# Optimization experiments

Measured on AMD Instinct MI355X. Metric: run time of the kernel, lower is better.

## Reference

```python
import jax, jax.numpy as jnp
import numpy as np

HEADS = 12
HEAD_SIZE = 64
INF = 1e12  # K.infinity() in bert4keras

B, L, D = 8, 1024, 768


def setup_inputs() -> dict:
    key = jax.random.key(0)
    k1, k2 = jax.random.split(key)
    x = jax.random.normal(k1, (B, L, D), dtype=jnp.float32)
    W = jax.random.normal(k2, (D, HEADS * HEAD_SIZE * 2), dtype=jnp.float32) * (1.0 / np.sqrt(D))
    b = jnp.zeros((HEADS * HEAD_SIZE * 2,), dtype=jnp.float32)
    mask = jnp.ones((B, L), dtype=jnp.int32)
    return {"x": x, "W": W, "b": b, "mask": mask}


def _rope_sin_cos(seq_len, head_size, dtype):
    # SinusoidalPositionEmbedding(head_size, 'zero'):
    # emb[n, 2i] = sin(n * 10000^(-2i/S)), emb[n, 2i+1] = cos(...)
    pos = jnp.arange(seq_len, dtype=dtype)                       # [L]
    inv = jnp.power(jnp.asarray(10000.0, dtype),
                    -2.0 * jnp.arange(head_size // 2, dtype=dtype) / head_size)  # [S/2]
    ang = pos[:, None] * inv[None, :]                            # [L, S/2]
    # repeat_elements(..., 2, -1): [c0,c0,c1,c1,...]
    cos_pos = jnp.repeat(jnp.cos(ang), 2, axis=-1)               # [L, S]
    sin_pos = jnp.repeat(jnp.sin(ang), 2, axis=-1)               # [L, S]
    return sin_pos[None, :, None, :], cos_pos[None, :, None, :]  # [1,L,1,S]


def _rotate_half_interleaved(t):
    # stack([-t[...,1::2], t[...,::2]], -1).reshape(t.shape)
    t2 = jnp.stack([-t[..., 1::2], t[..., ::2]], axis=-1)
    return t2.reshape(t.shape)


def reference(x, W, b, mask):
    dtype = x.dtype
    Bq, Lq, _ = x.shape
    S = HEAD_SIZE
    # dense projection + head split: [B, L, H, 2S]
    proj = (jnp.einsum('bld,de->ble', x, W) + b).reshape(Bq, Lq, HEADS, 2 * S)
    qw, kw = proj[..., :S], proj[..., S:]
    # inline RoPE (interleaved variant)
    sin_pos, cos_pos = _rope_sin_cos(Lq, S, dtype)
    qw = qw * cos_pos + _rotate_half_interleaved(qw) * sin_pos
    kw = kw * cos_pos + _rotate_half_interleaved(kw) * sin_pos
    # bilinear score: [B, H, L, L]
    logits = jnp.einsum('bmhd,bnhd->bhmn', qw, kw)
    # padding mask on axis 2 (rows) and axis 3 (cols): x*m + (-INF)*(1-m)
    m = mask.astype(dtype)
    m_row = m[:, None, :, None]
    m_col = m[:, None, None, :]
    logits = logits * m_row + (-INF) * (1.0 - m_row)
    logits = logits * m_col + (-INF) * (1.0 - m_col)
    # upper-triangular (incl. diagonal) mask
    tri = jnp.triu(jnp.ones((Lq, Lq), dtype=dtype))
    logits = logits - (1.0 - tri) * INF
    return logits / np.sqrt(S).astype(np.float32)
```

## Files before the change

### kernel.cpp

```cpp
#include <hip/hip_runtime.h>
#include <hip/hip_bf16.h>
#include <stdint.h>

#define NHEADS 12
#define HS 64
#define NB 8
#define NL 1024
#define ND 768
#define NE 1536
#define INFV 1000000000000.0f

typedef __bf16 bf16x8 __attribute__((ext_vector_type(8)));
typedef float f32x4 __attribute__((ext_vector_type(4)));

typedef __attribute__((address_space(1))) const unsigned int gas_uint;
typedef __attribute__((address_space(3))) unsigned int las_uint;
#define GLOAD_LDS16(g, l) __builtin_amdgcn_global_load_lds((gas_uint*)(g), (las_uint*)(l), 16, 0, 0)

__device__ __forceinline__ unsigned short f2bf(float f) {
  unsigned int u = __builtin_bit_cast(unsigned int, f);
  u += 0x7fffu + ((u >> 16) & 1u);
  return (unsigned short)(u >> 16);
}

__device__ __forceinline__ bf16x8 load_frag(const unsigned short* p) {
  uint4 v = *(const uint4*)p;
  return __builtin_bit_cast(bf16x8, v);
}

__global__ __launch_bounds__(256) void k_prep(
    const float* __restrict__ x, const float* __restrict__ W,
    unsigned short* __restrict__ xb, unsigned short* __restrict__ wt,
    float* __restrict__ cst) {
  const int blk = blockIdx.x;
  if (blk < 6144) {
    int i = blk * 256 + threadIdx.x;
    float4 v = ((const float4*)x)[i];
    ushort4 o;
    o.x = f2bf(v.x); o.y = f2bf(v.y); o.z = f2bf(v.z); o.w = f2bf(v.w);
    ((ushort4*)xb)[i] = o;
  } else if (blk < 6144 + 288) {
    __shared__ float tile[64][65];
    int t = blk - 6144;
    int te = t % 24, td = t / 24;
    int c = threadIdx.x & 63, r4 = threadIdx.x >> 6;
    #pragma unroll
    for (int rr = 0; rr < 16; rr++) {
      int row = rr * 4 + r4;
      tile[row][c] = W[(size_t)(td * 64 + row) * NE + te * 64 + c];
    }
    __syncthreads();
    #pragma unroll
    for (int rr = 0; rr < 16; rr++) {
      int row = rr * 4 + r4;
      wt[(size_t)(te * 64 + row) * ND + td * 64 + c] = f2bf(tile[c][row]);
    }
  } else {
    int t = (blk - 6432) * 256 + threadIdx.x;
    int p = t >> 5, i = t & 31;
    float inv = powf(10000.0f, -(float)i / 32.0f);
    float sv, cv;
    sincosf((float)p * inv, &sv, &cv);
    cst[(p * 32 + i) * 2 + 0] = cv;
    cst[(p * 32 + i) * 2 + 1] = sv;
  }
}

__global__ __launch_bounds__(256) void k_proj_rope(
    const unsigned short* __restrict__ xb,
    const unsigned short* __restrict__ wt,
    const float* __restrict__ bias,
    const float* __restrict__ cst,
    unsigned short* __restrict__ qbuf, unsigned short* __restrict__ kbuf) {
  const int h  = blockIdx.y;
  const int m0 = blockIdx.x * 128;
  const int e0 = h * 128;
  const int tid  = threadIdx.x;
  const int lane = tid & 63;
  const int w    = tid >> 6;
  const int wm = w >> 1, wn = w & 1;
  const int col_l = lane & 15, rq = lane >> 4;

  __shared__ unsigned short smem[16384];
  char* smem_b = (char*)smem;

  unsigned int goff[4], loff[4];
  #pragma unroll
  for (int q = 0; q < 4; q++) {
    int p  = q * 256 + tid;
    int r  = p >> 3, sl = p & 7;
    int s  = sl ^ (r & 7);
    goff[q] = r * ND + s * 8;
    loff[q] = p * 16;
  }
  const unsigned short* gA = wt + (size_t)e0 * ND;
  const unsigned short* gB = xb + (size_t)m0 * ND;

  const int xr = col_l & 7;
  const unsigned int aB0 = (unsigned)((wn * 64 + col_l) * 128 + ((0 * 4 + rq) ^ xr) * 16);
  const unsigned int aB1 = (unsigned)((wn * 64 + col_l) * 128 + ((1 * 4 + rq) ^ xr) * 16);
  const unsigned int bB0 = (unsigned)(16384 + (wm * 64 + col_l) * 128 + ((0 * 4 + rq) ^ xr) * 16);
  const unsigned int bB1 = (unsigned)(16384 + (wm * 64 + col_l) * 128 + ((1 * 4 + rq) ^ xr) * 16);

  f32x4 acc[4][4];
  #pragma unroll
  for (int i = 0; i < 4; i++)
    #pragma unroll
    for (int j = 0; j < 4; j++)
      #pragma unroll
      for (int q = 0; q < 4; q++) acc[i][j][q] = 0.0f;

  for (int kk = 0; kk < ND; kk += 64) {
    const unsigned short* sA = gA + kk;
    const unsigned short* sB = gB + kk;
    #pragma unroll
    for (int q = 0; q < 4; q++) GLOAD_LDS16(sA + goff[q], smem_b + loff[q]);
    #pragma unroll
    for (int q = 0; q < 4; q++) GLOAD_LDS16(sB + goff[q], smem_b + 16384 + loff[q]);
    __syncthreads();
    #pragma unroll
    for (int kkh = 0; kkh < 2; kkh++) {
      const unsigned int aB = kkh ? aB1 : aB0;
      const unsigned int bB = kkh ? bB1 : bB0;
      bf16x8 af[4], bfr[4];
      #pragma unroll
      for (int f = 0; f < 4; f++) {
        af[f]  = __builtin_bit_cast(bf16x8, *(const uint4*)(smem_b + aB + f * 2048));
        bfr[f] = __builtin_bit_cast(bf16x8, *(const uint4*)(smem_b + bB + f * 2048));
      }
      #pragma unroll
      for (int i = 0; i < 4; i++)
        #pragma unroll
        for (int j = 0; j < 4; j++)
          acc[i][j] = __builtin_amdgcn_mfma_f32_16x16x32_bf16(af[i], bfr[j], acc[i][j], 0, 0, 0);
    }
    __syncthreads();
  }

  unsigned short* obuf = (wn == 1) ? kbuf : qbuf;
  #pragma unroll
  for (int j = 0; j < 4; j++) {
    const int m   = m0 + wm * 64 + j * 16 + col_l;
    const int pos = m & (NL - 1);
    const int bb  = m >> 10;
    const float* crow = cst + pos * 64;
    unsigned short* orow = obuf + (((size_t)(bb * NHEADS + h)) * NL + pos) * HS;
    #pragma unroll
    for (int i = 0; i < 4; i++) {
      const int s0 = i * 16 + rq * 4;
      float4 bv = *(const float4*)&bias[e0 + wn * 64 + s0];
      float4 tq = *(const float4*)(crow + s0 * 2);
      float v0 = acc[i][j][0] + bv.x;
      float v1 = acc[i][j][1] + bv.y;
      float v2 = acc[i][j][2] + bv.z;
      float v3 = acc[i][j][3] + bv.w;
      ushort4 o;
      o.x = f2bf(v0 * tq.x - v1 * tq.y);
      o.y = f2bf(v1 * tq.x + v0 * tq.y);
      o.z = f2bf(v2 * tq.z - v3 * tq.w);
      o.w = f2bf(v3 * tq.z + v2 * tq.w);
      *(ushort4*)&orow[s0] = o;
    }
  }
}

__global__ __launch_bounds__(256) void k_logits(
    const unsigned short* __restrict__ qbuf,
    const unsigned short* __restrict__ kbuf,
    const int* __restrict__ mask,
    float* __restrict__ out) {
  const int f  = blockIdx.x;
  const int r  = f & 7, t = f >> 3;
  const int bh = r + 8 * (t >> 6);
  const int tile = t & 63;
  const int tm = tile >> 3, tn = tile & 7;
  const int b  = bh / NHEADS;
  const int tid  = threadIdx.x;
  const int* mrow = mask + b * NL;

  if (tn < tm) {
    const int n0 = tn * 128 + (tid & 31) * 4;
    int4 mc = *(const int4*)&mrow[n0];
    #pragma unroll
    for (int it = 0; it < 16; it++) {
      int m = tm * 128 + it * 8 + (tid >> 5);
      float mr = (float)mrow[m];
      float base = -INFV * (1.0f - mr);
      f32x4 o;
      o[0] = ((mc.x ? base : -INFV) - INFV) * 0.125f;
      o[1] = ((mc.y ? base : -INFV) - INFV) * 0.125f;
      o[2] = ((mc.z ? base : -INFV) - INFV) * 0.125f;
      o[3] = ((mc.w ? base : -INFV) - INFV) * 0.125f;
      __builtin_nontemporal_store(o, (f32x4*)(out + ((size_t)bh * NL + m) * NL + n0));
    }
    return;
  }

  const int lane = tid & 63;
  const int w    = tid >> 6;
  const int wm = w >> 1, wn = w & 1;
  const int m_base = tm * 128 + wm * 64;
  const int n_base = tn * 128 + wn * 64;
  const int col_l = lane & 15, rq = lane >> 4;
  const unsigned short* Q = qbuf + (size_t)bh * (NL * HS);
  const unsigned short* K = kbuf + (size_t)bh * (NL * HS);

  __shared__ float lds[64 * 132];

  f32x4 acc[4][4];
  #pragma unroll
  for (int i = 0; i < 4; i++)
    #pragma unroll
    for (int j = 0; j < 4; j++)
      #pragma unroll
      for (int q = 0; q < 4; q++) acc[i][j][q] = 0.0f;

  #pragma unroll
  for (int ks = 0; ks < 2; ks++) {
    bf16x8 ak[4], bq[4];
    #pragma unroll
    for (int ff = 0; ff < 4; ff++) {
      ak[ff] = load_frag(K + (size_t)(n_base + ff * 16 + col_l) * HS + ks * 32 + rq * 8);
      bq[ff] = load_frag(Q + (size_t)(m_base + ff * 16 + col_l) * HS + ks * 32 + rq * 8);
    }
    #pragma unroll
    for (int i = 0; i < 4; i++)
      #pragma unroll
      for (int j = 0; j < 4; j++)
        acc[i][j] = __builtin_amdgcn_mfma_f32_16x16x32_bf16(ak[i], bq[j], acc[i][j], 0, 0, 0);
  }

  const bool diag = (tn == tm);
  const int rb_row = tid >> 5;
  const int rb_c4  = (tid & 31) * 4;
  const int n_rb   = tn * 128 + rb_c4;
  int4 mc_rb = *(const int4*)&mrow[n_rb];
  const bool allmc = (mc_rb.x & mc_rb.y & mc_rb.z & mc_rb.w) != 0;

  #pragma unroll
  for (int pass = 0; pass < 2; pass++) {
    if (wm == pass) {
      #pragma unroll
      for (int j = 0; j < 4; j++) {
        const int rl = j * 16 + col_l;
        #pragma unroll
        for (int i = 0; i < 4; i++)
          *(f32x4*)&lds[rl * 132 + wn * 64 + i * 16 + rq * 4] = acc[i][j];
      }
    }
    __syncthreads();
    #pragma unroll
    for (int it = 0; it < 8; it++) {
      const int rl = it * 8 + rb_row;
      const int m  = tm * 128 + pass * 64 + rl;
      f32x4 v = *(const f32x4*)&lds[rl * 132 + rb_c4];
      if (mrow[m] == 0) { v[0] = -INFV; v[1] = -INFV; v[2] = -INFV; v[3] = -INFV; }
      if (!allmc) {
        if (mc_rb.x == 0) v[0] = -INFV;
        if (mc_rb.y == 0) v[1] = -INFV;
        if (mc_rb.z == 0) v[2] = -INFV;
        if (mc_rb.w == 0) v[3] = -INFV;
      }
      if (diag) {
        if (n_rb + 0 < m) v[0] -= INFV;
        if (n_rb + 1 < m) v[1] -= INFV;
        if (n_rb + 2 < m) v[2] -= INFV;
        if (n_rb + 3 < m) v[3] -= INFV;
      }
      v *= 0.125f;
      __builtin_nontemporal_store(v, (f32x4*)(out + ((size_t)bh * NL + m) * NL + n_rb));
    }
    __syncthreads();
  }
}

extern "C" void kernel_launch(void* const* d_in, const int* in_sizes, int n_in,
                              void* d_out, int out_size, void* d_ws, size_t ws_size,
                              hipStream_t stream) {
  const float* x    = (const float*)d_in[0];
  const float* W    = (const float*)d_in[1];
  const float* bias = (const float*)d_in[2];
  const int*   mask = (const int*)d_in[3];
  float* out = (float*)d_out;
  char* ws = (char*)d_ws;

  unsigned short* xb = (unsigned short*)(ws);
  unsigned short* wt = (unsigned short*)(ws + 12582912);
  unsigned short* qb = (unsigned short*)(ws + 14942208);
  unsigned short* kb = (unsigned short*)(ws + 27525120);
  float* cst = (float*)(ws + 40108032);

  k_prep<<<6560, 256, 0, stream>>>(x, W, xb, wt, cst);
  k_proj_rope<<<dim3(64, 12), 256, 0, stream>>>(xb, wt, bias, cst, qb, kb);
  k_logits<<<6144, 256, 0, stream>>>(qb, kb, mask, out);
}
```

Baseline: 127.8 us.

## Fuse fp32-to-bf16 conversion of x into projection GEMM with XCD-aware tile mapping

Removes the separate pass that converts x to bf16 in the prep kernel. The projection kernel now streams fp32 x tiles straight into a larger swizzled LDS buffer and converts them to bf16 as it builds the MFMA fragments. The grid becomes 1D and is remapped so the 12 head tiles that share the same rows of x land on the same XCD, which should improve L2 reuse of the wider fp32 loads. The RoPE cos/sin table index is also corrected. The cost is more global and LDS traffic per GEMM tile, plus conversion work inside the inner loop.

```diff
diff --git a/kernel.cpp b/kernel.cpp
--- a/kernel.cpp
+++ b/kernel.cpp
@@ -29,20 +29,13 @@
 }
 
 __global__ __launch_bounds__(256) void k_prep(
-    const float* __restrict__ x, const float* __restrict__ W,
-    unsigned short* __restrict__ xb, unsigned short* __restrict__ wt,
+    const float* __restrict__ W,
+    unsigned short* __restrict__ wt,
     float* __restrict__ cst) {
   const int blk = blockIdx.x;
-  if (blk < 6144) {
-    int i = blk * 256 + threadIdx.x;
-    float4 v = ((const float4*)x)[i];
-    ushort4 o;
-    o.x = f2bf(v.x); o.y = f2bf(v.y); o.z = f2bf(v.z); o.w = f2bf(v.w);
-    ((ushort4*)xb)[i] = o;
-  } else if (blk < 6144 + 288) {
+  if (blk < 288) {
     __shared__ float tile[64][65];
-    int t = blk - 6144;
-    int te = t % 24, td = t / 24;
+    int te = blk % 24, td = blk / 24;
     int c = threadIdx.x & 63, r4 = threadIdx.x >> 6;
     #pragma unroll
     for (int rr = 0; rr < 16; rr++) {
@@ -56,7 +49,7 @@
       wt[(size_t)(te * 64 + row) * ND + td * 64 + c] = f2bf(tile[c][row]);
     }
   } else {
-    int t = (blk - 6432) * 256 + threadIdx.x;
+    int t = (blk - 288) * 256 + threadIdx.x;
     int p = t >> 5, i = t & 31;
     float inv = powf(10000.0f, -(float)i / 32.0f);
     float sv, cv;
@@ -67,40 +60,46 @@
 }
 
 __global__ __launch_bounds__(256) void k_proj_rope(
-    const unsigned short* __restrict__ xb,
+    const float* __restrict__ x,
     const unsigned short* __restrict__ wt,
     const float* __restrict__ bias,
     const float* __restrict__ cst,
     unsigned short* __restrict__ qbuf, unsigned short* __restrict__ kbuf) {
-  const int h  = blockIdx.y;
-  const int m0 = blockIdx.x * 128;
-  const int e0 = h * 128;
+  const int blk = blockIdx.x;
+  const int xcd = blk & 7;
+  const int loc = blk >> 3;
+  const int h   = loc % 12;
+  const int mt  = xcd * 8 + loc / 12;
+  const int m0  = mt * 128;
+  const int e0  = h * 128;
   const int tid  = threadIdx.x;
   const int lane = tid & 63;
   const int w    = tid >> 6;
   const int wm = w >> 1, wn = w & 1;
   const int col_l = lane & 15, rq = lane >> 4;
 
-  __shared__ unsigned short smem[16384];
-  char* smem_b = (char*)smem;
-
-  unsigned int goff[4], loff[4];
+  __shared__ char smem_b[49152];
+
+  unsigned int goffA[4];
   #pragma unroll
   for (int q = 0; q < 4; q++) {
-    int p  = q * 256 + tid;
-    int r  = p >> 3, sl = p & 7;
-    int s  = sl ^ (r & 7);
-    goff[q] = r * ND + s * 8;
-    loff[q] = p * 16;
+    int p = q * 256 + tid;
+    int r = p >> 3, sl = p & 7;
+    goffA[q] = r * ND + (sl ^ (r & 7)) * 8;
+  }
+  unsigned int goffB[8];
+  #pragma unroll
+  for (int q = 0; q < 8; q++) {
+    int p = q * 256 + tid;
+    int r = p >> 4, sl = p & 15;
+    goffB[q] = r * ND + (sl ^ (r & 15)) * 4;
   }
   const unsigned short* gA = wt + (size_t)e0 * ND;
-  const unsigned short* gB = xb + (size_t)m0 * ND;
+  const float*          gB = x  + (size_t)m0 * ND;
 
   const int xr = col_l & 7;
-  const unsigned int aB0 = (unsigned)((wn * 64 + col_l) * 128 + ((0 * 4 + rq) ^ xr) * 16);
-  const unsigned int aB1 = (unsigned)((wn * 64 + col_l) * 128 + ((1 * 4 + rq) ^ xr) * 16);
-  const unsigned int bB0 = (unsigned)(16384 + (wm * 64 + col_l) * 128 + ((0 * 4 + rq) ^ xr) * 16);
-  const unsigned int bB1 = (unsigned)(16384 + (wm * 64 + col_l) * 128 + ((1 * 4 + rq) ^ xr) * 16);
+  const unsigned int aRow = (unsigned)((wn * 64 + col_l) * 128);
+  const unsigned int bRow = (unsigned)(16384 + (wm * 64 + col_l) * 256);
 
   f32x4 acc[4][4];
   #pragma unroll
@@ -112,21 +111,24 @@
 
   for (int kk = 0; kk < ND; kk += 64) {
     const unsigned short* sA = gA + kk;
-    const unsigned short* sB = gB + kk;
-    #pragma unroll
-    for (int q = 0; q < 4; q++) GLOAD_LDS16(sA + goff[q], smem_b + loff[q]);
-    #pragma unroll
-    for (int q = 0; q < 4; q++) GLOAD_LDS16(sB + goff[q], smem_b + 16384 + loff[q]);
+    const float*          sB = gB + kk;
+    #pragma unroll
+    for (int q = 0; q < 4; q++) GLOAD_LDS16(sA + goffA[q], smem_b + (q * 256 + tid) * 16);
+    #pragma unroll
+    for (int q = 0; q < 8; q++) GLOAD_LDS16(sB + goffB[q], smem_b + 16384 + (q * 256 + tid) * 16);
     __syncthreads();
     #pragma unroll
     for (int kkh = 0; kkh < 2; kkh++) {
-      const unsigned int aB = kkh ? aB1 : aB0;
-      const unsigned int bB = kkh ? bB1 : bB0;
       bf16x8 af[4], bfr[4];
       #pragma unroll
       for (int f = 0; f < 4; f++) {
-        af[f]  = __builtin_bit_cast(bf16x8, *(const uint4*)(smem_b + aB + f * 2048));
-        bfr[f] = __builtin_bit_cast(bf16x8, *(const uint4*)(smem_b + bB + f * 2048));
+        af[f] = __builtin_bit_cast(bf16x8,
+            *(const uint4*)(smem_b + aRow + f * 2048 + (((kkh << 2) | rq) ^ xr) * 16));
+        const int sl0 = (kkh << 3) | (rq << 1);
+        float4 lo = *(const float4*)(smem_b + bRow + f * 4096 + ((sl0 ^ col_l) * 16));
+        float4 hi = *(const float4*)(smem_b + bRow + f * 4096 + (((sl0 + 1) ^ col_l) * 16));
+        bfr[f] = bf16x8{(__bf16)lo.x, (__bf16)lo.y, (__bf16)lo.z, (__bf16)lo.w,
+                        (__bf16)hi.x, (__bf16)hi.y, (__bf16)hi.z, (__bf16)hi.w};
       }
       #pragma unroll
       for (int i = 0; i < 4; i++)
@@ -149,7 +151,7 @@
     for (int i = 0; i < 4; i++) {
       const int s0 = i * 16 + rq * 4;
       float4 bv = *(const float4*)&bias[e0 + wn * 64 + s0];
-      float4 tq = *(const float4*)(crow + s0 * 2);
+      float4 tq = *(const float4*)(crow + s0);
       float v0 = acc[i][j][0] + bv.x;
       float v1 = acc[i][j][1] + bv.y;
       float v2 = acc[i][j][2] + bv.z;
@@ -284,13 +286,12 @@
   float* out = (float*)d_out;
   char* ws = (char*)d_ws;
 
-  unsigned short* xb = (unsigned short*)(ws);
-  unsigned short* wt = (unsigned short*)(ws + 12582912);
-  unsigned short* qb = (unsigned short*)(ws + 14942208);
-  unsigned short* kb = (unsigned short*)(ws + 27525120);
-  float* cst = (float*)(ws + 40108032);
-
-  k_prep<<<6560, 256, 0, stream>>>(x, W, xb, wt, cst);
-  k_proj_rope<<<dim3(64, 12), 256, 0, stream>>>(xb, wt, bias, cst, qb, kb);
+  unsigned short* wt = (unsigned short*)(ws);
+  unsigned short* qb = (unsigned short*)(ws + 2359296);
+  unsigned short* kb = (unsigned short*)(ws + 14942208);
+  float* cst = (float*)(ws + 27525120);
+
+  k_prep<<<416, 256, 0, stream>>>(W, wt, cst);
+  k_proj_rope<<<768, 256, 0, stream>>>(x, wt, bias, cst, qb, kb);
   k_logits<<<6144, 256, 0, stream>>>(qb, kb, mask, out);
 }
```

New measurement: 129.5 us. No clear change (+1.3%).
